# Optimization experiments

Measured on AMD Instinct MI355X. Metric: run time of the kernel, lower is better.

The kernel has to match this reference:

```python
import jax, jax.numpy as jnp
import numpy as np

WS = 8        # window_size
HEAD_DIM = 32
KEYS = ["ln1_g", "ln1_b", "qkv_w", "qkv_b", "rpb", "proj_w", "proj_b",
        "ln2_g", "ln2_b", "w1", "b1", "w2", "b2"]


def _rel_bias(rpb, ws):
    # rpb: [h, 2ws-1, 2ws-1] -> bias [h, P, P] via relative coordinates
    coords = np.stack(np.meshgrid(np.arange(ws), np.arange(ws), indexing='ij'), -1).reshape(-1, 2)
    rel = coords[:, None, :] - coords[None, :, :] + ws - 1  # [P,P,2]
    return rpb[:, rel[..., 0], rel[..., 1]]


def _sw_mask(nh, nw, p, shift):
    # boolean mask [nW, P, P]; True = masked (cross-segment after cyclic shift)
    m = np.zeros((nh, nw, p, p, p, p), dtype=bool)
    s = p - shift
    m[-1, :, :s, :, s:, :] = True
    m[-1, :, s:, :, :s, :] = True
    m[:, -1, :, :s, :, s:] = True
    m[:, -1, :, s:, :, :s] = True
    return jnp.asarray(m.reshape(nh * nw, p * p, p * p))


def _ln(x, g, b):
    mu = x.mean(-1, keepdims=True)
    var = ((x - mu) ** 2).mean(-1, keepdims=True)
    return (x - mu) / jnp.sqrt(var + 1e-5) * g + b


def _wmsa(x, qkv_w, qkv_b, rpb, proj_w, proj_b, shifted):
    B, H, W, C = x.shape
    ws, hd = WS, HEAD_DIM
    h = C // hd
    shift = ws // 2
    if shifted:
        x = jnp.roll(x, (-shift, -shift), axis=(1, 2))
    nh, nw = H // ws, W // ws
    # window partition: [B, nW, P, C]
    xw = x.reshape(B, nh, ws, nw, ws, C).transpose(0, 1, 3, 2, 4, 5).reshape(B, nh * nw, ws * ws, C)
    qkv = xw @ qkv_w + qkv_b                               # [B,nW,P,3C]
    qkv = qkv.reshape(B, nh * nw, ws * ws, 3, h, hd)       # (3h,c) split -> first h heads = q
    q, k, v = qkv[..., 0, :, :], qkv[..., 1, :, :], qkv[..., 2, :, :]
    sim = jnp.einsum('bwphd,bwqhd->bhwpq', q, k) * (hd ** -0.5)
    sim = sim + _rel_bias(rpb, ws)[None, :, None]
    if shifted:
        mask = _sw_mask(nh, nw, ws, shift)                 # [nW,P,P]
        sim = jnp.where(mask[None, None], -jnp.inf, sim)
    probs = jax.nn.softmax(sim, axis=-1)
    out = jnp.einsum('bhwpq,bwqhd->bwphd', probs, v).reshape(B, nh * nw, ws * ws, C)
    out = out @ proj_w + proj_b
    out = out.reshape(B, nh, nw, ws, ws, C).transpose(0, 1, 3, 2, 4, 5).reshape(B, H, W, C)
    if shifted:
        out = jnp.roll(out, (shift, shift), axis=(1, 2))
    return out


def _block(x, p, shifted):
    x = x + _wmsa(_ln(x, p['ln1_g'], p['ln1_b']), p['qkv_w'], p['qkv_b'], p['rpb'],
                  p['proj_w'], p['proj_b'], shifted)
    y = _ln(x, p['ln2_g'], p['ln2_b'])
    y = jax.nn.gelu(y @ p['w1'] + p['b1'], approximate=False) @ p['w2'] + p['b2']
    return x + y


def setup_inputs() -> dict:
    B, C, H, W = 2, 192, 256, 256
    h = C // HEAD_DIM
    key = jax.random.key(0)
    ks = jax.random.split(key, 11)
    n = lambda k, shape: jax.random.normal(k, shape, jnp.float32) * 0.02
    inp = {"x": jax.random.normal(ks[0], (B, C, H, W), jnp.float32)}
    for i, pre in enumerate(("b1_", "b2_")):
        o = 1 + i * 5
        inp[pre + "ln1_g"] = jnp.ones((C,), jnp.float32)
        inp[pre + "ln1_b"] = jnp.zeros((C,), jnp.float32)
        inp[pre + "qkv_w"] = n(ks[o], (C, 3 * C))
        inp[pre + "qkv_b"] = jnp.zeros((3 * C,), jnp.float32)
        inp[pre + "rpb"] = n(ks[o + 1], (h, 2 * WS - 1, 2 * WS - 1))
        inp[pre + "proj_w"] = n(ks[o + 2], (C, C))
        inp[pre + "proj_b"] = jnp.zeros((C,), jnp.float32)
        inp[pre + "ln2_g"] = jnp.ones((C,), jnp.float32)
        inp[pre + "ln2_b"] = jnp.zeros((C,), jnp.float32)
        inp[pre + "w1"] = n(ks[o + 3], (C, 4 * C))
        inp[pre + "b1"] = jnp.zeros((4 * C,), jnp.float32)
        inp[pre + "w2"] = n(ks[o + 4], (4 * C, C))
        inp[pre + "b2"] = jnp.zeros((C,), jnp.float32)
    return inp


def reference(x, b1_ln1_g, b1_ln1_b, b1_qkv_w, b1_qkv_b, b1_rpb, b1_proj_w, b1_proj_b,
              b1_ln2_g, b1_ln2_b, b1_w1, b1_b1, b1_w2, b1_b2,
              b2_ln1_g, b2_ln1_b, b2_qkv_w, b2_qkv_b, b2_rpb, b2_proj_w, b2_proj_b,
              b2_ln2_g, b2_ln2_b, b2_w1, b2_b1, b2_w2, b2_b2):
    p1 = dict(zip(KEYS, (b1_ln1_g, b1_ln1_b, b1_qkv_w, b1_qkv_b, b1_rpb, b1_proj_w, b1_proj_b,
                         b1_ln2_g, b1_ln2_b, b1_w1, b1_b1, b1_w2, b1_b2)))
    p2 = dict(zip(KEYS, (b2_ln1_g, b2_ln1_b, b2_qkv_w, b2_qkv_b, b2_rpb, b2_proj_w, b2_proj_b,
                         b2_ln2_g, b2_ln2_b, b2_w1, b2_b1, b2_w2, b2_b2)))
    t = jnp.transpose(x, (0, 2, 3, 1))   # b c h w -> b h w c
    t = _block(t, p1, shifted=False)     # W block
    t = _block(t, p2, shifted=True)      # SW block
    return jnp.transpose(t, (0, 3, 1, 2))  # b h w c -> b c h w
```

## Files before the change

### kernel.cpp

```cpp
#include <hip/hip_runtime.h>
#include <math.h>

typedef unsigned short u16;
typedef u16 u16x8 __attribute__((ext_vector_type(8)));
typedef __bf16 bf16x8 __attribute__((ext_vector_type(8)));
typedef float f32x4 __attribute__((ext_vector_type(4)));

__device__ __forceinline__ u16 f2bf(float f) {
    union { float f; unsigned u; } v; v.f = f;
    unsigned r = v.u + 0x7fffu + ((v.u >> 16) & 1u);
    return (u16)(r >> 16);
}

__device__ __forceinline__ void gload16(const void* g, void* l) {
    __builtin_amdgcn_global_load_lds((const __attribute__((address_space(1))) void*)g,
                                     (__attribute__((address_space(3))) void*)l,
                                     16, 0, 0);
}

__device__ __forceinline__ float redsum16(float s) {
    s += __shfl_xor(s, 1, 64);
    s += __shfl_xor(s, 2, 64);
    s += __shfl_xor(s, 4, 64);
    s += __shfl_xor(s, 8, 64);
    return s;
}

__global__ __launch_bounds__(256) void tl_k(const float* __restrict__ in,
                                            const float* __restrict__ g,
                                            const float* __restrict__ b,
                                            float* __restrict__ xbuf,
                                            u16* __restrict__ lnbuf) {
    __shared__ float T[192][33];
    __shared__ float MU[32], RS[32];
    const int t = threadIdx.x;
    const int bid = blockIdx.x;
    const int bb = bid >> 11;
    const int s0 = (bid & 2047) * 32;
    const float* src = in + (size_t)bb * 192 * 65536 + s0;
    const int sx = t & 31, cg = t >> 5;
#pragma unroll
    for (int i = 0; i < 24; i++) {
        int c = cg + i * 8;
        T[c][sx] = src[(size_t)c * 65536 + sx];
    }
    __syncthreads();
    {
        const int tok = t >> 3, sub = t & 7;
        float s = 0.f;
#pragma unroll
        for (int i = 0; i < 24; i++) s += T[sub + i * 8][tok];
        s += __shfl_xor(s, 1, 64); s += __shfl_xor(s, 2, 64); s += __shfl_xor(s, 4, 64);
        float mu = s * (1.f / 192.f);
        float q = 0.f;
#pragma unroll
        for (int i = 0; i < 24; i++) { float d = T[sub + i * 8][tok] - mu; q += d * d; }
        q += __shfl_xor(q, 1, 64); q += __shfl_xor(q, 2, 64); q += __shfl_xor(q, 4, 64);
        if (sub == 0) { MU[tok] = mu; RS[tok] = rsqrtf(q * (1.f / 192.f) + 1e-5f); }
    }
    __syncthreads();
    const size_t tokG0 = (size_t)bb * 65536 + s0;
#pragma unroll
    for (int i = 0; i < 3; i++) {
        int chunk = i * 256 + t;
        int tk = chunk / 24;
        int c0 = (chunk - tk * 24) * 8;
        float mu = MU[tk], rs = RS[tk];
        f32x4 g0 = *(const f32x4*)&g[c0], g1 = *(const f32x4*)&g[c0 + 4];
        f32x4 b0 = *(const f32x4*)&b[c0], b1 = *(const f32x4*)&b[c0 + 4];
        u16x8 ov;
#pragma unroll
        for (int e = 0; e < 4; e++) ov[e] = f2bf((T[c0 + e][tk] - mu) * rs * g0[e] + b0[e]);
#pragma unroll
        for (int e = 0; e < 4; e++) ov[e + 4] = f2bf((T[c0 + 4 + e][tk] - mu) * rs * g1[e] + b1[e]);
        *(u16x8*)&lnbuf[(tokG0 + tk) * 192 + c0] = ov;
    }
#pragma unroll
    for (int i = 0; i < 6; i++) {
        int chunk = i * 256 + t;
        int tk = chunk / 48;
        int c0 = (chunk - tk * 48) * 4;
        f32x4 v;
#pragma unroll
        for (int e = 0; e < 4; e++) v[e] = T[c0 + e][tk];
        *(f32x4*)&xbuf[(tokG0 + tk) * 192 + c0] = v;
    }
}

__global__ __launch_bounds__(256) void transpose_out(const float* __restrict__ in,
                                                     float* __restrict__ out) {
    __shared__ float t[32][33];
    const int b = blockIdx.z;
    const int c0 = blockIdx.y * 32;
    const int s0 = blockIdx.x * 32;
    const int tx = threadIdx.x, ty = threadIdx.y;
    const float* src = in + (size_t)b * 65536 * 192;
    float* dst = out + (size_t)b * 192 * 65536;
#pragma unroll
    for (int k = 0; k < 4; k++)
        t[ty + k * 8][tx] = src[(size_t)(s0 + ty + k * 8) * 192 + c0 + tx];
    __syncthreads();
#pragma unroll
    for (int k = 0; k < 4; k++)
        dst[(size_t)(c0 + ty + k * 8) * 65536 + s0 + tx] = t[tx][ty + k * 8];
}

__global__ __launch_bounds__(256) void wtrans(const float* __restrict__ w,
                                              u16* __restrict__ wt, int K, int N) {
    int idx = blockIdx.x * 256 + threadIdx.x;
    if (idx >= K * N) return;
    int n = idx / K, k = idx % K;
    wt[idx] = f2bf(w[(size_t)k * N + n]);
}

template <int ACT>
__global__ __launch_bounds__(256, 3) void gemm_small(const u16* __restrict__ A,
                                                     const u16* __restrict__ Wt,
                                                     const float* __restrict__ bias,
                                                     u16* __restrict__ outb,
                                                     int N, int Nb) {
    __shared__ __align__(16) u16 Bs[64 * 192];
    const int t = threadIdx.x, l = t & 63, w = t >> 6;
    const int nwg = gridDim.x, q8 = nwg >> 3;
    const int wg = (blockIdx.x & 7) * q8 + (blockIdx.x >> 3);
    const int bn = wg % Nb, bm = wg / Nb;
    const size_t m0 = (size_t)bm * 128;
    const int n0 = bn * 64;
    const int lc = l & 15, lg = l >> 4;

#pragma unroll
    for (int r = 0; r < 6; r++) {
        int f = r * 2048 + t * 8;
        int row = f / 192;
        int c = ((f - row * 192) >> 3) ^ (row & 7);
        gload16(Wt + (size_t)(n0 + row) * 192 + c * 8, &Bs[f]);
    }
    const u16* ga = A + (m0 + w * 32 + lc) * 192 + lg * 8;
    bf16x8 af[6][2];
#pragma unroll
    for (int ks = 0; ks < 6; ks++)
#pragma unroll
        for (int tm = 0; tm < 2; tm++)
            af[ks][tm] = *(const bf16x8*)(ga + tm * 3072 + ks * 32);

    f32x4 acc[2][4] = {};
    __syncthreads();
#pragma unroll
    for (int ks = 0; ks < 6; ks++) {
        bf16x8 bfr[4];
#pragma unroll
        for (int tn = 0; tn < 4; tn++) {
            int row = tn * 16 + lc;
            int p = (ks * 4 + lg) ^ (row & 7);
            bfr[tn] = *(const bf16x8*)&Bs[row * 192 + p * 8];
        }
#pragma unroll
        for (int tm = 0; tm < 2; tm++)
#pragma unroll
            for (int tn = 0; tn < 4; tn++)
                acc[tm][tn] = __builtin_amdgcn_mfma_f32_16x16x32_bf16(af[ks][tm], bfr[tn],
                                                                     acc[tm][tn], 0, 0, 0);
    }
    float bv[4];
#pragma unroll
    for (int tn = 0; tn < 4; tn++) bv[tn] = bias[n0 + tn * 16 + lc];
    __syncthreads();
    u16* Ct = Bs;
#pragma unroll
    for (int tm = 0; tm < 2; tm++)
#pragma unroll
        for (int tn = 0; tn < 4; tn++)
#pragma unroll
            for (int r = 0; r < 4; r++) {
                int row = w * 32 + tm * 16 + (lg << 2) + r;
                float v = acc[tm][tn][r] + bv[tn];
                Ct[row * 72 + tn * 16 + lc] = f2bf(v);
            }
    __syncthreads();
#pragma unroll
    for (int i = 0; i < 4; i++) {
        int row = i * 32 + (t >> 3), seg = t & 7;
        *(u16x8*)&outb[(m0 + row) * (size_t)N + n0 + seg * 8] =
            *(const u16x8*)&Ct[row * 72 + seg * 8];
    }
}

__global__ __launch_bounds__(512, 2) void proj_ln_k(const u16* __restrict__ A,
                                                    const u16* __restrict__ Wt,
                                                    const float* __restrict__ bias,
                                                    float* __restrict__ res,
                                                    const float* __restrict__ g,
                                                    const float* __restrict__ b,
                                                    u16* __restrict__ lnout) {
    __shared__ __align__(16) u16 Bs[192 * 192];
    const int t = threadIdx.x, l = t & 63, w = t >> 6;
    const size_t m0 = (size_t)blockIdx.x * 256;
    const int lc = l & 15, lg = l >> 4;
#pragma unroll
    for (int r = 0; r < 9; r++) {
        int f = r * 4096 + t * 8;
        int row = f / 192;
        int c = ((f - row * 192) >> 3) ^ (row & 7);
        gload16(Wt + (size_t)row * 192 + c * 8, &Bs[f]);
    }
    const u16* ga = A + (m0 + w * 32 + lc) * 192 + lg * 8;
    bf16x8 af[6][2];
#pragma unroll
    for (int ks = 0; ks < 6; ks++)
#pragma unroll
        for (int tm = 0; tm < 2; tm++)
            af[ks][tm] = *(const bf16x8*)(ga + tm * 3072 + ks * 32);

    f32x4 acc[2][12] = {};
    __syncthreads();
#pragma unroll
    for (int ks = 0; ks < 6; ks++) {
        bf16x8 bfr[12];
#pragma unroll
        for (int tn = 0; tn < 12; tn++) {
            int row = tn * 16 + lc;
            int p = (ks * 4 + lg) ^ (row & 7);
            bfr[tn] = *(const bf16x8*)&Bs[row * 192 + p * 8];
        }
#pragma unroll
        for (int tm = 0; tm < 2; tm++)
#pragma unroll
            for (int tn = 0; tn < 12; tn++)
                acc[tm][tn] = __builtin_amdgcn_mfma_f32_16x16x32_bf16(af[ks][tm], bfr[tn],
                                                                     acc[tm][tn], 0, 0, 0);
    }
    float bv[12], gv[12], bb[12];
#pragma unroll
    for (int tn = 0; tn < 12; tn++) {
        bv[tn] = bias[tn * 16 + lc];
        gv[tn] = g[tn * 16 + lc];
        bb[tn] = b[tn * 16 + lc];
    }
#pragma unroll
    for (int tm = 0; tm < 2; tm++)
#pragma unroll
        for (int r = 0; r < 4; r++) {
            int row = w * 32 + tm * 16 + (lg << 2) + r;
            size_t base = (m0 + row) * 192;
            float v[12], s = 0.f;
#pragma unroll
            for (int tn = 0; tn < 12; tn++) {
                v[tn] = acc[tm][tn][r] + bv[tn] + res[base + tn * 16 + lc];
                s += v[tn];
            }
            s = redsum16(s);
            float mu = s * (1.f / 192.f);
            float q = 0.f;
#pragma unroll
            for (int tn = 0; tn < 12; tn++) { float d = v[tn] - mu; q += d * d; }
            q = redsum16(q);
            float rstd = rsqrtf(q * (1.f / 192.f) + 1e-5f);
#pragma unroll
            for (int tn = 0; tn < 12; tn++) {
                res[base + tn * 16 + lc] = v[tn];
                lnout[base + tn * 16 + lc] = f2bf((v[tn] - mu) * rstd * gv[tn] + bb[tn]);
            }
        }
}

template <int DO_LN>
__global__ __launch_bounds__(512, 4) void mlp_fused(const u16* __restrict__ A,
                                                    const u16* __restrict__ W1t,
                                                    const float* __restrict__ b1,
                                                    const u16* __restrict__ W2t,
                                                    const float* __restrict__ b2,
                                                    float* __restrict__ res,
                                                    const float* __restrict__ g,
                                                    const float* __restrict__ bl,
                                                    u16* __restrict__ lnout) {
    __shared__ __align__(16) u16 W1s[2][32 * 192];
    __shared__ __align__(16) u16 W2s[2][192 * 32];
    __shared__ __align__(16) u16 Is[128 * 32];
    const int t = threadIdx.x, l = t & 63, w = t >> 6;
    const int nwg = gridDim.x, q8 = nwg >> 3;
    const int wg = (blockIdx.x & 7) * q8 + (blockIdx.x >> 3);
    const size_t m0 = (size_t)wg * 128;
    const int lc = l & 15, lg = l >> 4;

    const u16* ga = A + (m0 + w * 16 + lc) * 192 + lg * 8;
    bf16x8 af[6];
#pragma unroll
    for (int ks = 0; ks < 6; ks++) af[ks] = *(const bf16x8*)(ga + ks * 32);

#define STAGE(bufi, c)                                                            \
    do {                                                                          \
        _Pragma("unroll") for (int i = 0; i < 3; i++) {                           \
            int cid = i * 512 + t;                                                \
            if (cid < 768) {                                                      \
                int f = cid * 8;                                                  \
                int row = f / 192;                                                \
                int cw = ((f - row * 192) >> 3) ^ (row & 7);                      \
                gload16(W1t + ((size_t)(c) * 32 + row) * 192 + cw * 8,            \
                        &W1s[bufi][f]);                                           \
            } else {                                                              \
                int f = (cid - 768) * 8;                                          \
                int row = f >> 5;                                                 \
                int cw = ((f >> 3) & 3) ^ ((row >> 1) & 3);                       \
                gload16(W2t + (size_t)row * 768 + (c) * 32 + cw * 8,              \
                        &W2s[bufi][f]);                                           \
            }                                                                     \
        }                                                                         \
    } while (0)

    f32x4 acc2[12] = {};
    STAGE(0, 0);
    __syncthreads();
#pragma unroll 1
    for (int c = 0; c < 24; c++) {
        const int buf = c & 1;
        if (c < 23) STAGE(buf ^ 1, c + 1);
        f32x4 a1[2] = {};
#pragma unroll
        for (int ks = 0; ks < 6; ks++) {
            bf16x8 bfr[2];
#pragma unroll
            for (int tn = 0; tn < 2; tn++) {
                int row = tn * 16 + lc;
                int p = (ks * 4 + lg) ^ (row & 7);
                bfr[tn] = *(const bf16x8*)&W1s[buf][row * 192 + p * 8];
            }
#pragma unroll
            for (int tn = 0; tn < 2; tn++)
                a1[tn] = __builtin_amdgcn_mfma_f32_16x16x32_bf16(af[ks], bfr[tn],
                                                                 a1[tn], 0, 0, 0);
        }
        float b1v[2];
#pragma unroll
        for (int tn = 0; tn < 2; tn++) b1v[tn] = b1[c * 32 + tn * 16 + lc];
#pragma unroll
        for (int tn = 0; tn < 2; tn++)
#pragma unroll
            for (int r = 0; r < 4; r++) {
                int row = w * 16 + (lg << 2) + r;
                int col = tn * 16 + lc;
                float x = a1[tn][r] + b1v[tn];
                float y2 = 1.5957691216057308f * (x + 0.044715f * x * x * x);
                float v = x / (1.0f + __expf(-y2));
                int cw = (col >> 3) ^ ((row >> 1) & 3);
                Is[row * 32 + cw * 8 + (col & 7)] = f2bf(v);
            }
        bf16x8 a2;
        {
            int row = w * 16 + lc;
            int ch = lg ^ ((row >> 1) & 3);
            a2 = *(const bf16x8*)&Is[row * 32 + ch * 8];
        }
#pragma unroll
        for (int grp = 0; grp < 2; grp++) {
            bf16x8 b2f[6];
#pragma unroll
            for (int tn = 0; tn < 6; tn++) {
                int row = (grp * 6 + tn) * 16 + lc;
                int ch = lg ^ ((row >> 1) & 3);
                b2f[tn] = *(const bf16x8*)&W2s[buf][row * 32 + ch * 8];
            }
#pragma unroll
            for (int tn = 0; tn < 6; tn++)
                acc2[grp * 6 + tn] = __builtin_amdgcn_mfma_f32_16x16x32_bf16(a2, b2f[tn],
                                                                            acc2[grp * 6 + tn], 0, 0, 0);
        }
        __syncthreads();
    }
#undef STAGE
    float bv[12];
#pragma unroll
    for (int tn = 0; tn < 12; tn++) bv[tn] = b2[tn * 16 + lc];
    float gv[12], bb[12];
    if (DO_LN) {
#pragma unroll
        for (int tn = 0; tn < 12; tn++) { gv[tn] = g[tn * 16 + lc]; bb[tn] = bl[tn * 16 + lc]; }
    }
#pragma unroll
    for (int r = 0; r < 4; r++) {
        int row = w * 16 + (lg << 2) + r;
        size_t base = (m0 + row) * 192;
        float v[12], s = 0.f;
#pragma unroll
        for (int tn = 0; tn < 12; tn++) {
            v[tn] = acc2[tn][r] + bv[tn] + res[base + tn * 16 + lc];
            s += v[tn];
        }
#pragma unroll
        for (int tn = 0; tn < 12; tn++) res[base + tn * 16 + lc] = v[tn];
        if (DO_LN) {
            s = redsum16(s);
            float mu = s * (1.f / 192.f);
            float q = 0.f;
#pragma unroll
            for (int tn = 0; tn < 12; tn++) { float d = v[tn] - mu; q += d * d; }
            q = redsum16(q);
            float rstd = rsqrtf(q * (1.f / 192.f) + 1e-5f);
#pragma unroll
            for (int tn = 0; tn < 12; tn++)
                lnout[base + tn * 16 + lc] = f2bf((v[tn] - mu) * rstd * gv[tn] + bb[tn]);
        }
    }
}

__global__ __launch_bounds__(64) void attn_k(const u16* __restrict__ qkv,
                                             const float* __restrict__ rpb,
                                             u16* __restrict__ aout, int shifted) {
    __shared__ __align__(16) u16 Vt[32][72];
    __shared__ __align__(16) u16 Ps[64][72];
    const int l = threadIdx.x;
    const int head = blockIdx.x;
    const int wy = blockIdx.y;
    const int b = wy >> 10, widx = wy & 1023;
    const int wh = widx >> 5, ww = widx & 31;
    const int soff = shifted ? 4 : 0;
    const int lc = l & 15;
    const int lg = l >> 4;

    {
        int i1 = l >> 3, j1 = l & 7;
        int hh = (wh * 8 + i1 + soff) & 255;
        int wc = (ww * 8 + j1 + soff) & 255;
        const u16* base = qkv + (((size_t)b * 256 + hh) * 256 + wc) * 576 + head * 32 + 384;
#pragma unroll
        for (int s = 0; s < 4; s++) {
            u16x8 v = *(const u16x8*)(base + s * 8);
#pragma unroll
            for (int e = 0; e < 8; e++) Vt[s * 8 + e][l] = v[e];
        }
    }

    bf16x8 qa[4], kb[4];
#pragma unroll
    for (int tm = 0; tm < 4; tm++) {
        int p = tm * 16 + lc;
        int pi = p >> 3, pj = p & 7;
        int hh = (wh * 8 + pi + soff) & 255;
        int wc = (ww * 8 + pj + soff) & 255;
        const u16* tp = qkv + (((size_t)b * 256 + hh) * 256 + wc) * 576 + head * 32;
        qa[tm] = *(const bf16x8*)(tp + lg * 8);
        kb[tm] = *(const bf16x8*)(tp + 192 + lg * 8);
    }

    f32x4 acc[4][4] = {};
    __builtin_amdgcn_s_setprio(1);
#pragma unroll
    for (int tm = 0; tm < 4; tm++)
#pragma unroll
        for (int tn = 0; tn < 4; tn++)
            acc[tm][tn] = __builtin_amdgcn_mfma_f32_16x16x32_bf16(qa[tm], kb[tn], acc[tm][tn], 0, 0, 0);
    __builtin_amdgcn_s_setprio(0);

    const float scale = 0.17677669529663687f;
    const float* rp = rpb + head * 225;
#pragma unroll
    for (int tm = 0; tm < 4; tm++) {
#pragma unroll
        for (int r = 0; r < 4; r++) {
            int p = tm * 16 + (lg << 2) + r;
            int pi = p >> 3, pj = p & 7;
            float sv[4];
#pragma unroll
            for (int tn = 0; tn < 4; tn++) {
                int qq = tn * 16 + lc;
                int qi = qq >> 3, qj = qq & 7;
                float xv = acc[tm][tn][r] * scale + rp[(pi - qi + 7) * 15 + (pj - qj + 7)];
                if (shifted) {
                    bool msk = (wh == 31 && ((pi < 4) != (qi < 4))) ||
                               (ww == 31 && ((pj < 4) != (qj < 4)));
                    if (msk) xv = -1e30f;
                }
                sv[tn] = xv;
            }
            float mx = fmaxf(fmaxf(sv[0], sv[1]), fmaxf(sv[2], sv[3]));
#pragma unroll
            for (int m = 1; m < 16; m <<= 1) mx = fmaxf(mx, __shfl_xor(mx, m, 64));
            float sum = 0.f;
#pragma unroll
            for (int tn = 0; tn < 4; tn++) { sv[tn] = __expf(sv[tn] - mx); sum += sv[tn]; }
#pragma unroll
            for (int m = 1; m < 16; m <<= 1) sum += __shfl_xor(sum, m, 64);
            float inv = 1.0f / sum;
#pragma unroll
            for (int tn = 0; tn < 4; tn++) Ps[p][tn * 16 + lc] = f2bf(sv[tn] * inv);
        }
    }
    __syncthreads();

    f32x4 o[4][2] = {};
    {
        bf16x8 pa[4], vb[2];
#pragma unroll
        for (int kk = 0; kk < 2; kk++) {
#pragma unroll
            for (int tm = 0; tm < 4; tm++) pa[tm] = *(const bf16x8*)&Ps[tm * 16 + lc][kk * 32 + lg * 8];
#pragma unroll
            for (int tn = 0; tn < 2; tn++) vb[tn] = *(const bf16x8*)&Vt[tn * 16 + lc][kk * 32 + lg * 8];
            __builtin_amdgcn_s_setprio(1);
#pragma unroll
            for (int tm = 0; tm < 4; tm++)
#pragma unroll
                for (int tn = 0; tn < 2; tn++)
                    o[tm][tn] = __builtin_amdgcn_mfma_f32_16x16x32_bf16(pa[tm], vb[tn], o[tm][tn], 0, 0, 0);
            __builtin_amdgcn_s_setprio(0);
        }
    }
#pragma unroll
    for (int tm = 0; tm < 4; tm++)
#pragma unroll
        for (int r = 0; r < 4; r++) {
            int p = tm * 16 + (lg << 2) + r;
            int pi = p >> 3, pj = p & 7;
            int h2 = (wh * 8 + pi + soff) & 255;
            int w2 = (ww * 8 + pj + soff) & 255;
            size_t t2 = ((size_t)b * 256 + h2) * 256 + w2;
#pragma unroll
            for (int tn = 0; tn < 2; tn++)
                aout[t2 * 192 + head * 32 + tn * 16 + lc] = f2bf(o[tm][tn][r]);
        }
}

extern "C" void kernel_launch(void* const* d_in, const int* in_sizes, int n_in,
                              void* d_out, int out_size, void* d_ws, size_t ws_size,
                              hipStream_t stream) {
    (void)in_sizes; (void)n_in; (void)out_size; (void)ws_size;
    const float* x_in = (const float*)d_in[0];

    char* ws = (char*)d_ws;
    float* xbuf = (float*)ws;
    u16* lnbuf = (u16*)(ws + 100663296);
    u16* big   = (u16*)(ws + 150994944);
    u16* wts   = (u16*)(ws + 352321536);

    u16* qkvt[2]; u16* projt[2]; u16* w1t[2]; u16* w2t[2];
    for (int bi = 0; bi < 2; bi++) {
        size_t base = (size_t)bi * 442368;
        qkvt[bi]  = wts + base;
        projt[bi] = wts + base + 110592;
        w1t[bi]   = wts + base + 147456;
        w2t[bi]   = wts + base + 294912;
    }

    for (int bi = 0; bi < 2; bi++) {
        const int base = 1 + bi * 13;
        wtrans<<<dim3((110592 + 255) / 256), 256, 0, stream>>>((const float*)d_in[base + 2],  qkvt[bi],  192, 576);
        wtrans<<<dim3((36864  + 255) / 256), 256, 0, stream>>>((const float*)d_in[base + 5],  projt[bi], 192, 192);
        wtrans<<<dim3((147456 + 255) / 256), 256, 0, stream>>>((const float*)d_in[base + 9],  w1t[bi],   192, 768);
        wtrans<<<dim3((147456 + 255) / 256), 256, 0, stream>>>((const float*)d_in[base + 11], w2t[bi],   768, 192);
    }

    tl_k<<<4096, 256, 0, stream>>>(x_in, (const float*)d_in[1], (const float*)d_in[2], xbuf, lnbuf);

    for (int bi = 0; bi < 2; bi++) {
        const int base = 1 + bi * 13;
        const float* qkv_b  = (const float*)d_in[base + 3];
        const float* rpb    = (const float*)d_in[base + 4];
        const float* proj_b = (const float*)d_in[base + 6];
        const float* ln2_g  = (const float*)d_in[base + 7];
        const float* ln2_b  = (const float*)d_in[base + 8];
        const float* b1     = (const float*)d_in[base + 10];
        const float* b2     = (const float*)d_in[base + 12];

        gemm_small<0><<<9216, 256, 0, stream>>>(lnbuf, qkvt[bi], qkv_b, big, 576, 9);
        attn_k<<<dim3(6, 2048), 64, 0, stream>>>(big, rpb, lnbuf, bi);
        proj_ln_k<<<512, 512, 0, stream>>>(lnbuf, projt[bi], proj_b, xbuf, ln2_g, ln2_b, lnbuf);
        if (bi == 0) {
            mlp_fused<1><<<1024, 512, 0, stream>>>(lnbuf, w1t[bi], b1, w2t[bi], b2, xbuf,
                                                   (const float*)d_in[14], (const float*)d_in[15], lnbuf);
        } else {
            mlp_fused<0><<<1024, 512, 0, stream>>>(lnbuf, w1t[bi], b1, w2t[bi], b2, xbuf,
                                                   nullptr, nullptr, nullptr);
        }
    }

    transpose_out<<<dim3(2048, 6, 2), dim3(32, 8), 0, stream>>>(xbuf, (float*)d_out);
}
```

Baseline: 834.2 us.

## Raise occupancy of proj and MLP kernels by shrinking tiles and LDS

```diff
diff --git a/kernel.cpp b/kernel.cpp
--- a/kernel.cpp
+++ b/kernel.cpp
@@ -114,7 +114,7 @@
 }
 
 template <int ACT>
-__global__ __launch_bounds__(256, 3) void gemm_small(const u16* __restrict__ A,
+__global__ __launch_bounds__(256, 4) void gemm_small(const u16* __restrict__ A,
                                                      const u16* __restrict__ Wt,
                                                      const float* __restrict__ bias,
                                                      u16* __restrict__ outb,
@@ -185,7 +185,7 @@
     }
 }
 
-__global__ __launch_bounds__(512, 2) void proj_ln_k(const u16* __restrict__ A,
+__global__ __launch_bounds__(512, 4) void proj_ln_k(const u16* __restrict__ A,
                                                     const u16* __restrict__ Wt,
                                                     const float* __restrict__ bias,
                                                     float* __restrict__ res,
@@ -194,7 +194,7 @@
                                                     u16* __restrict__ lnout) {
     __shared__ __align__(16) u16 Bs[192 * 192];
     const int t = threadIdx.x, l = t & 63, w = t >> 6;
-    const size_t m0 = (size_t)blockIdx.x * 256;
+    const size_t m0 = (size_t)blockIdx.x * 128;
     const int lc = l & 15, lg = l >> 4;
 #pragma unroll
     for (int r = 0; r < 9; r++) {
@@ -203,31 +203,29 @@
         int c = ((f - row * 192) >> 3) ^ (row & 7);
         gload16(Wt + (size_t)row * 192 + c * 8, &Bs[f]);
     }
-    const u16* ga = A + (m0 + w * 32 + lc) * 192 + lg * 8;
-    bf16x8 af[6][2];
-#pragma unroll
-    for (int ks = 0; ks < 6; ks++)
-#pragma unroll
-        for (int tm = 0; tm < 2; tm++)
-            af[ks][tm] = *(const bf16x8*)(ga + tm * 3072 + ks * 32);
-
-    f32x4 acc[2][12] = {};
+    const u16* ga = A + (m0 + w * 16 + lc) * 192 + lg * 8;
+    bf16x8 af[6];
+#pragma unroll
+    for (int ks = 0; ks < 6; ks++) af[ks] = *(const bf16x8*)(ga + ks * 32);
+
+    f32x4 acc[12] = {};
     __syncthreads();
 #pragma unroll
     for (int ks = 0; ks < 6; ks++) {
-        bf16x8 bfr[12];
-#pragma unroll
-        for (int tn = 0; tn < 12; tn++) {
-            int row = tn * 16 + lc;
-            int p = (ks * 4 + lg) ^ (row & 7);
-            bfr[tn] = *(const bf16x8*)&Bs[row * 192 + p * 8];
-        }
-#pragma unroll
-        for (int tm = 0; tm < 2; tm++)
-#pragma unroll
-            for (int tn = 0; tn < 12; tn++)
-                acc[tm][tn] = __builtin_amdgcn_mfma_f32_16x16x32_bf16(af[ks][tm], bfr[tn],
-                                                                     acc[tm][tn], 0, 0, 0);
+#pragma unroll
+        for (int grp = 0; grp < 3; grp++) {
+            bf16x8 bfr[4];
+#pragma unroll
+            for (int tn = 0; tn < 4; tn++) {
+                int row = (grp * 4 + tn) * 16 + lc;
+                int p = (ks * 4 + lg) ^ (row & 7);
+                bfr[tn] = *(const bf16x8*)&Bs[row * 192 + p * 8];
+            }
+#pragma unroll
+            for (int tn = 0; tn < 4; tn++)
+                acc[grp * 4 + tn] = __builtin_amdgcn_mfma_f32_16x16x32_bf16(af[ks], bfr[tn],
+                                                                            acc[grp * 4 + tn], 0, 0, 0);
+        }
     }
     float bv[12], gv[12], bb[12];
 #pragma unroll
@@ -237,34 +235,32 @@
         bb[tn] = b[tn * 16 + lc];
     }
 #pragma unroll
-    for (int tm = 0; tm < 2; tm++)
-#pragma unroll
-        for (int r = 0; r < 4; r++) {
-            int row = w * 32 + tm * 16 + (lg << 2) + r;
-            size_t base = (m0 + row) * 192;
-            float v[12], s = 0.f;
-#pragma unroll
-            for (int tn = 0; tn < 12; tn++) {
-                v[tn] = acc[tm][tn][r] + bv[tn] + res[base + tn * 16 + lc];
-                s += v[tn];
-            }
-            s = redsum16(s);
-            float mu = s * (1.f / 192.f);
-            float q = 0.f;
-#pragma unroll
-            for (int tn = 0; tn < 12; tn++) { float d = v[tn] - mu; q += d * d; }
-            q = redsum16(q);
-            float rstd = rsqrtf(q * (1.f / 192.f) + 1e-5f);
-#pragma unroll
-            for (int tn = 0; tn < 12; tn++) {
-                res[base + tn * 16 + lc] = v[tn];
-                lnout[base + tn * 16 + lc] = f2bf((v[tn] - mu) * rstd * gv[tn] + bb[tn]);
-            }
-        }
+    for (int r = 0; r < 4; r++) {
+        int row = w * 16 + (lg << 2) + r;
+        size_t base = (m0 + row) * 192;
+        float v[12], s = 0.f;
+#pragma unroll
+        for (int tn = 0; tn < 12; tn++) {
+            v[tn] = acc[tn][r] + bv[tn] + res[base + tn * 16 + lc];
+            s += v[tn];
+        }
+        s = redsum16(s);
+        float mu = s * (1.f / 192.f);
+        float q = 0.f;
+#pragma unroll
+        for (int tn = 0; tn < 12; tn++) { float d = v[tn] - mu; q += d * d; }
+        q = redsum16(q);
+        float rstd = rsqrtf(q * (1.f / 192.f) + 1e-5f);
+#pragma unroll
+        for (int tn = 0; tn < 12; tn++) {
+            res[base + tn * 16 + lc] = v[tn];
+            lnout[base + tn * 16 + lc] = f2bf((v[tn] - mu) * rstd * gv[tn] + bb[tn]);
+        }
+    }
 }
 
 template <int DO_LN>
-__global__ __launch_bounds__(512, 4) void mlp_fused(const u16* __restrict__ A,
+__global__ __launch_bounds__(512, 6) void mlp_fused(const u16* __restrict__ A,
                                                     const u16* __restrict__ W1t,
                                                     const float* __restrict__ b1,
                                                     const u16* __restrict__ W2t,
@@ -273,7 +269,7 @@
                                                     const float* __restrict__ g,
                                                     const float* __restrict__ bl,
                                                     u16* __restrict__ lnout) {
-    __shared__ __align__(16) u16 W1s[2][32 * 192];
+    __shared__ __align__(16) u16 W1s[32 * 192];
     __shared__ __align__(16) u16 W2s[2][192 * 32];
     __shared__ __align__(16) u16 Is[128 * 32];
     const int t = threadIdx.x, l = t & 63, w = t >> 6;
@@ -287,33 +283,42 @@
 #pragma unroll
     for (int ks = 0; ks < 6; ks++) af[ks] = *(const bf16x8*)(ga + ks * 32);
 
-#define STAGE(bufi, c)                                                            \
-    do {                                                                          \
-        _Pragma("unroll") for (int i = 0; i < 3; i++) {                           \
-            int cid = i * 512 + t;                                                \
-            if (cid < 768) {                                                      \
-                int f = cid * 8;                                                  \
-                int row = f / 192;                                                \
-                int cw = ((f - row * 192) >> 3) ^ (row & 7);                      \
-                gload16(W1t + ((size_t)(c) * 32 + row) * 192 + cw * 8,            \
-                        &W1s[bufi][f]);                                           \
-            } else {                                                              \
-                int f = (cid - 768) * 8;                                          \
-                int row = f >> 5;                                                 \
-                int cw = ((f >> 3) & 3) ^ ((row >> 1) & 3);                       \
-                gload16(W2t + (size_t)row * 768 + (c) * 32 + cw * 8,              \
-                        &W2s[bufi][f]);                                           \
-            }                                                                     \
-        }                                                                         \
+#define STW1(c)                                                               \
+    do {                                                                      \
+        int f = t * 8;                                                        \
+        int row = f / 192;                                                    \
+        int cw = ((f - row * 192) >> 3) ^ (row & 7);                          \
+        gload16(W1t + ((size_t)(c) * 32 + row) * 192 + cw * 8, &W1s[f]);      \
+        if (t < 256) {                                                        \
+            int f2 = (512 + t) * 8;                                           \
+            int row2 = f2 / 192;                                              \
+            int cw2 = ((f2 - row2 * 192) >> 3) ^ (row2 & 7);                  \
+            gload16(W1t + ((size_t)(c) * 32 + row2) * 192 + cw2 * 8,          \
+                    &W1s[f2]);                                                \
+        }                                                                     \
     } while (0)
+#define STW2(bufi, c)                                                         \
+    do {                                                                      \
+        int f = t * 8;                                                        \
+        int row = f >> 5;                                                     \
+        int cw = ((f >> 3) & 3) ^ ((row >> 1) & 3);                           \
+        gload16(W2t + (size_t)row * 768 + (c) * 32 + cw * 8, &W2s[bufi][f]);  \
+        if (t < 256) {                                                        \
+            int f2 = (512 + t) * 8;                                           \
+            int row2 = f2 >> 5;                                               \
+            int cw2 = ((f2 >> 3) & 3) ^ ((row2 >> 1) & 3);                    \
+            gload16(W2t + (size_t)row2 * 768 + (c) * 32 + cw2 * 8,            \
+                    &W2s[bufi][f2]);                                          \
+        }                                                                     \
+    } while (0)
 
     f32x4 acc2[12] = {};
-    STAGE(0, 0);
+    STW1(0);
+    STW2(0, 0);
     __syncthreads();
 #pragma unroll 1
     for (int c = 0; c < 24; c++) {
         const int buf = c & 1;
-        if (c < 23) STAGE(buf ^ 1, c + 1);
         f32x4 a1[2] = {};
 #pragma unroll
         for (int ks = 0; ks < 6; ks++) {
@@ -322,7 +327,7 @@
             for (int tn = 0; tn < 2; tn++) {
                 int row = tn * 16 + lc;
                 int p = (ks * 4 + lg) ^ (row & 7);
-                bfr[tn] = *(const bf16x8*)&W1s[buf][row * 192 + p * 8];
+                bfr[tn] = *(const bf16x8*)&W1s[row * 192 + p * 8];
             }
 #pragma unroll
             for (int tn = 0; tn < 2; tn++)
@@ -339,11 +344,14 @@
                 int row = w * 16 + (lg << 2) + r;
                 int col = tn * 16 + lc;
                 float x = a1[tn][r] + b1v[tn];
-                float y2 = 1.5957691216057308f * (x + 0.044715f * x * x * x);
-                float v = x / (1.0f + __expf(-y2));
+                float u = x * x;
+                float y = x * fmaf(-0.07136031f, u, -1.5957691f);
+                float v = x * __builtin_amdgcn_rcpf(1.0f + __expf(y));
                 int cw = (col >> 3) ^ ((row >> 1) & 3);
                 Is[row * 32 + cw * 8 + (col & 7)] = f2bf(v);
             }
+        __syncthreads();
+        if (c < 23) { STW1(c + 1); STW2(buf ^ 1, c + 1); }
         bf16x8 a2;
         {
             int row = w * 16 + lc;
@@ -366,7 +374,8 @@
         }
         __syncthreads();
     }
-#undef STAGE
+#undef STW1
+#undef STW2
     float bv[12];
 #pragma unroll
     for (int tn = 0; tn < 12; tn++) bv[tn] = b2[tn * 16 + lc];
@@ -562,7 +571,7 @@
 
         gemm_small<0><<<9216, 256, 0, stream>>>(lnbuf, qkvt[bi], qkv_b, big, 576, 9);
         attn_k<<<dim3(6, 2048), 64, 0, stream>>>(big, rpb, lnbuf, bi);
-        proj_ln_k<<<512, 512, 0, stream>>>(lnbuf, projt[bi], proj_b, xbuf, ln2_g, ln2_b, lnbuf);
+        proj_ln_k<<<1024, 512, 0, stream>>>(lnbuf, projt[bi], proj_b, xbuf, ln2_g, ln2_b, lnbuf);
         if (bi == 0) {
             mlp_fused<1><<<1024, 512, 0, stream>>>(lnbuf, w1t[bi], b1, w2t[bi], b2, xbuf,
                                                    (const float*)d_in[14], (const float*)d_in[15], lnbuf);
```

New measurement: 1.398 ms. 1.68x slower.
